# Performance work log

Measured on AMD Instinct MI355X. Metric: run time of the kernel, lower is better.

The kernel has to match this reference:

```python
import jax, jax.numpy as jnp
import numpy as np

EPS = 1e-6
HID = 2048; N_HEADS = 16; Q_LORA = 768; KV_LORA = 512
ROPE_D = 64; NOPE_D = 128; V_D = 128
IDX_H = 32; IDX_D = 128; IDX_TOPK = 512
N_EXP = 8; TOPK = 4; N_GROUP = 4; TOPK_GROUP = 2
MOE_I = 512; SHARED_I = 512; ROUTED_SCALE = 2.5
T = 1024
NEG = -1e30


def _rms(x, w, eps=EPS):
    x = x.astype(jnp.float32)
    return x * jax.lax.rsqrt(jnp.mean(x * x, axis=-1, keepdims=True) + eps) * w


def _ln(x, w, b, eps=EPS):
    x = x.astype(jnp.float32)
    m = jnp.mean(x, axis=-1, keepdims=True)
    v = jnp.mean((x - m) ** 2, axis=-1, keepdims=True)
    return (x - m) * jax.lax.rsqrt(v + eps) * w + b


def _rope_cs(positions, dim):
    inv = 1.0 / (10000.0 ** (jnp.arange(0, dim, 2, dtype=jnp.float32) / dim))
    f = positions.astype(jnp.float32)[:, None] * inv[None, :]  # [T, dim/2]
    return jnp.cos(f), jnp.sin(f)


def _rope(x, cos, sin):
    # neox-style rotate-half over last dim
    d = x.shape[-1] // 2
    x1, x2 = x[..., :d], x[..., d:]
    while cos.ndim < x.ndim:
        cos, sin = cos[:, None], sin[:, None]
    return jnp.concatenate([x1 * cos - x2 * sin, x2 * cos + x1 * sin], axis=-1)


def setup_inputs() -> dict:
    key = jax.random.key(0)
    ks = iter(jax.random.split(key, 32))
    w = lambda *s: jax.random.normal(next(ks), s, jnp.float32) * 0.02
    inp = {
        'positions': jnp.arange(T, dtype=jnp.int32),
        'hidden_states': jax.random.normal(next(ks), (T, HID), jnp.float32),
        'residual': jax.random.normal(next(ks), (T, HID), jnp.float32),
        'w_input_ln': jnp.ones((HID,), jnp.float32),
        'w_post_ln': jnp.ones((HID,), jnp.float32),
        'w_step1': w(Q_LORA + KV_LORA + ROPE_D + IDX_D + IDX_H, HID),
        'w_q_a_ln': jnp.ones((Q_LORA,), jnp.float32),
        'w_kv_a_ln': jnp.ones((KV_LORA,), jnp.float32),
        'idx_k_ln_w': jnp.ones((IDX_D,), jnp.float32),
        'idx_k_ln_b': jnp.zeros((IDX_D,), jnp.float32),
        'w_step3': w(IDX_H * IDX_D + N_HEADS * (NOPE_D + ROPE_D), Q_LORA),
        'W_UK_T': w(N_HEADS, NOPE_D, KV_LORA),
        'W_UV': w(N_HEADS, KV_LORA, V_D),
        'w_o': w(HID, N_HEADS * V_D),
        'gate_w': w(N_EXP, HID),
        'gate_bias': jnp.zeros((N_EXP,), jnp.float32),
        'shared_gate_up': w(2 * SHARED_I, HID),
        'shared_down': w(HID, SHARED_I),
        'exp_gate_up': w(N_EXP, 2 * MOE_I, HID),
        'exp_down': w(N_EXP, HID, MOE_I),
    }
    return inp


def reference(positions, hidden_states, residual, w_input_ln, w_post_ln, w_step1,
              w_q_a_ln, w_kv_a_ln, idx_k_ln_w, idx_k_ln_b, w_step3, W_UK_T, W_UV,
              w_o, gate_w, gate_bias, shared_gate_up, shared_down, exp_gate_up, exp_down):
    Tn = hidden_states.shape[0]
    rows = jnp.arange(Tn)
    # (allreduce is identity at tp=1) + residual add + RMSNorm
    res = hidden_states.astype(jnp.float32) + residual.astype(jnp.float32)
    h = _rms(res, w_input_ln)
    # ---- Step 1: fused qkv_a + indexer_wk + indexer_weights_proj GEMM ----
    s1 = h @ w_step1.T
    o0 = 0
    q_c = s1[:, o0:o0 + Q_LORA]; o0 += Q_LORA
    kv_c = s1[:, o0:o0 + KV_LORA]; o0 += KV_LORA
    k_pe = s1[:, o0:o0 + ROPE_D]; o0 += ROPE_D
    idx_k = s1[:, o0:o0 + IDX_D]; o0 += IDX_D
    idx_w_raw = s1[:, o0:o0 + IDX_H]
    cos, sin = _rope_cs(positions, ROPE_D)
    # fused_norm_rope: norms + rope on k_pe / indexer-k
    q_c = _rms(q_c, w_q_a_ln)
    kv_c = _rms(kv_c, w_kv_a_ln)
    k_pe = _rope(k_pe, cos, sin)
    idx_k = _ln(idx_k, idx_k_ln_w, idx_k_ln_b)
    idx_k = jnp.concatenate([_rope(idx_k[:, :ROPE_D], cos, sin), idx_k[:, ROPE_D:]], axis=-1)
    # ---- Step 3: fused indexer_wq_b + q_b_proj GEMM ----
    s3 = q_c @ w_step3.T
    idx_q = s3[:, :IDX_H * IDX_D].reshape(Tn, IDX_H, IDX_D)
    q = s3[:, IDX_H * IDX_D:].reshape(Tn, N_HEADS, NOPE_D + ROPE_D)
    q_nope, q_pe = q[..., :NOPE_D], q[..., NOPE_D:]
    # absorb W_UK: [T,H,nope] x [H,nope,kv_lora] -> [T,H,kv_lora]
    ql_nope = jnp.einsum('thn,hnk->thk', q_nope, W_UK_T)
    q_pe = _rope(q_pe, cos, sin)
    idx_q = jnp.concatenate([_rope(idx_q[..., :ROPE_D], cos, sin), idx_q[..., ROPE_D:]], axis=-1)
    idx_q = idx_q * (IDX_D ** -0.5)            # indexer softmax scale
    idx_w = idx_w_raw * (IDX_H ** -0.5)        # per-head weights scale
    # ---- sparse attention indexer: relu(q.k) head-weighted sum, causal top-k ----
    il = jnp.einsum('thd,sd->ths', idx_q, idx_k)          # [T,Hi,S]
    iscores = jnp.einsum('ths,th->ts', jax.nn.relu(il), idx_w)
    causal = positions[:, None] >= positions[None, :]
    iscores = jnp.where(causal, iscores, NEG)
    topk_idx = jax.lax.top_k(iscores, IDX_TOPK)[1]        # [T, IDX_TOPK]
    tmask = jnp.zeros((Tn, Tn), bool).at[rows[:, None], topk_idx].set(True)
    mask = causal & tmask
    # ---- MLA MQA attention in latent space ----
    mqa_q = jnp.concatenate([ql_nope, jnp.broadcast_to(q_pe, (Tn, N_HEADS, ROPE_D))], axis=-1)
    kv = jnp.concatenate([kv_c, k_pe], axis=-1)           # [S, kv_lora+rope]
    att = jnp.einsum('thd,sd->hts', mqa_q, kv) * ((NOPE_D + ROPE_D) ** -0.5)
    att = jnp.where(mask[None], att, NEG)
    p = jax.nn.softmax(att, axis=-1)
    o = jnp.einsum('hts,sk->thk', p, kv_c)                # [T,H,kv_lora]
    o = jnp.einsum('thk,hkv->thv', o, W_UV).reshape(Tn, N_HEADS * V_D)
    attn_out = o @ w_o.T
    # add + RMSNorm
    res2 = attn_out + res
    h2 = _rms(res2, w_post_ln)
    # ---- MoE: DeepSeekV3 sigmoid grouped routing + shared experts ----
    glog = h2 @ gate_w.T
    sg = jax.nn.sigmoid(glog)
    sc = sg + gate_bias
    gsz = N_EXP // N_GROUP
    grp = sc.reshape(Tn, N_GROUP, gsz)
    grp_score = jax.lax.top_k(grp, min(2, gsz))[0].sum(-1)
    gidx = jax.lax.top_k(grp_score, TOPK_GROUP)[1]
    gmask = jnp.zeros((Tn, N_GROUP), bool).at[rows[:, None], gidx].set(True)
    emask = jnp.repeat(gmask, gsz, axis=1)
    sc_m = jnp.where(emask, sc, NEG)
    _, tid = jax.lax.top_k(sc_m, TOPK)
    tw = jnp.take_along_axis(sg, tid, axis=1)
    tw = tw / (tw.sum(-1, keepdims=True) + 1e-20) * ROUTED_SCALE
    comb = jnp.zeros((Tn, N_EXP), jnp.float32).at[rows[:, None], tid].set(tw)
    # routed experts (dense masked combine as reference for grouped-GEMM dispatch)
    gu = jnp.einsum('th,eih->tei', h2, exp_gate_up)       # [T,E,2I]
    act = jax.nn.silu(gu[..., :MOE_I]) * gu[..., MOE_I:]
    routed_e = jnp.einsum('tei,ehi->teh', act, exp_down)  # [T,E,H]
    routed = jnp.einsum('te,teh->th', comb, routed_e)
    # shared experts
    gus = h2 @ shared_gate_up.T
    shared = (jax.nn.silu(gus[:, :SHARED_I]) * gus[:, SHARED_I:]) @ shared_down.T
    out = shared + routed
    return out, res2
```

## Files before the change

kernel.cpp:

```cpp
#include <hip/hip_runtime.h>
#include <math.h>

static constexpr int TT  = 1024;
static constexpr int HID = 2048;
static constexpr int NH  = 16;
static constexpr int QL  = 768;
static constexpr int KVL = 512;
static constexpr int RD  = 64;
static constexpr int IH  = 32;
static constexpr int ID  = 128;
static constexpr int S1W = QL + KVL + RD + ID + IH;
static constexpr int S3W = IH*ID + NH*(128+RD);

#define SCALE_ATT 0.07216878364870323f
#define SC_IDXQ   0.08838834764831845f
#define SC_IDXW   0.17677669529663687f
#define NEGR      -1e30f
#define NEGL      -3.0e38f

typedef __bf16 bf16x8 __attribute__((ext_vector_type(8)));
typedef float  f32x4  __attribute__((ext_vector_type(4)));

__device__ __forceinline__ unsigned short f2b(float x) {
  union { float f; unsigned u; } v; v.f = x;
// ... 24 lines not shown
  float vals[8]; float ss = 0.f;
  #pragma unroll
  for (int r = 0; r < 8; r++) {
    int d = threadIdx.x + 256*r;
    float v = hs[(size_t)t*HID + d] + rsd[(size_t)t*HID + d];
    vals[r] = v; res[(size_t)t*HID + d] = v; ss = fmaf(v, v, ss);
  }
  ss = blk_sum256(ss, scr);
  float inv = 1.f/sqrtf(ss/(float)HID + 1e-6f);
  #pragma unroll
  for (int r = 0; r < 8; r++) {
    int d = threadIdx.x + 256*r;
    hb[(size_t)t*HID + d] = f2b(vals[r]*inv*w[d]);
  }
}

__global__ __launch_bounds__(256) void k_res2(const float* __restrict__ attn1,
                                              const float* __restrict__ attn2,
                                              const float* __restrict__ res,
                                              const float* __restrict__ w,
                                              float* __restrict__ res2_out,
                                              float* __restrict__ h2,
                                              unsigned short* __restrict__ h2b) {
  int t = blockIdx.x;
  __shared__ float scr[4];
  float vals[8]; float ss = 0.f;
  #pragma unroll
  for (int r = 0; r < 8; r++) {
    int d = threadIdx.x + 256*r;
    float v = attn1[(size_t)t*HID + d] + attn2[(size_t)t*HID + d] + res[(size_t)t*HID + d];
    vals[r] = v; res2_out[(size_t)t*HID + d] = v; ss = fmaf(v, v, ss);
  }
  ss = blk_sum256(ss, scr);
  float inv = 1.f/sqrtf(ss/(float)HID + 1e-6f);
  #pragma unroll
  for (int r = 0; r < 8; r++) {
    int d = threadIdx.x + 256*r;
    float o = vals[r]*inv*w[d];
    h2[(size_t)t*HID + d] = o;
    h2b[(size_t)t*HID + d] = f2b(o);
  }
}

__global__ void k_ropecs(const int* __restrict__ pos, float* __restrict__ cosb, float* __restrict__ sinb) {
  int i = blockIdx.x*256 + threadIdx.x;
  if (i >= TT*32) return;
  int t = i >> 5, k = i & 31;
  double inv = pow(10000.0, -((double)(2*k))/64.0);
  double f = (double)pos[t] * inv;
  cosb[i] = (float)cos(f);
  sinb[i] = (float)sin(f);
}

__global__ void k_f2b(const float* __restrict__ s, unsigned short* __restrict__ d,
                      long long n, long long ntot) {
  long long stride = (long long)gridDim.x * 1024;
  for (long long i = ((long long)blockIdx.x*256 + threadIdx.x)*4; i < ntot; i += stride) {
    float x0, x1, x2, x3;
    if (i + 3 < n) { float4 v = *(const float4*)(s + i); x0=v.x; x1=v.y; x2=v.z; x3=v.w; }
    else {
      x0 = (i   < n) ? s[i]   : 0.f; x1 = (i+1 < n) ? s[i+1] : 0.f;
      x2 = (i+2 < n) ? s[i+2] : 0.f; x3 = (i+3 < n) ? s[i+3] : 0.f;
    }
    ushort4 o; o.x=f2b(x0); o.y=f2b(x1); o.z=f2b(x2); o.w=f2b(x3);
    *(ushort4*)(d + i) = o;
  }
}

__global__ void k_f2b4(const float* __restrict__ s0, unsigned short* __restrict__ d0, long long n0,
                       const float* __restrict__ s1, unsigned short* __restrict__ d1, long long n1,
                       const float* __restrict__ s2, unsigned short* __restrict__ d2, long long n2,
                       const float* __restrict__ s3, unsigned short* __restrict__ d3, long long n3) {
  long long ntot = n0 + n1 + n2 + n3;
  long long stride = (long long)gridDim.x * 1024;
  for (long long i = ((long long)blockIdx.x*256 + threadIdx.x)*4; i < ntot; i += stride) {
    const float* s; unsigned short* d; long long j = i;
    if (j < n0) { s = s0; d = d0; }
    else { j -= n0;
      if (j < n1) { s = s1; d = d1; }
      else { j -= n1;
        if (j < n2) { s = s2; d = d2; }
        else { j -= n2; s = s3; d = d3; } } }
    float4 v = *(const float4*)(s + j);
    ushort4 o; o.x=f2b(v.x); o.y=f2b(v.y); o.z=f2b(v.z); o.w=f2b(v.w);
    *(ushort4*)(d + j) = o;
  }
}

__global__ __launch_bounds__(256) void k_tconvb(const float* __restrict__ src,
                                                unsigned short* __restrict__ dst,
                                                int R, int C) {
  src += (size_t)blockIdx.z * R * C;
  dst += (size_t)blockIdx.z * R * C;
  __shared__ float tile[32][33];
  int c0 = blockIdx.x * 32, r0 = blockIdx.y * 32;
  int tx = threadIdx.x & 31, ty = threadIdx.x >> 5;
  #pragma unroll
  for (int i = 0; i < 4; i++) {
    int r = r0 + ty + i*8;
    tile[ty + i*8][tx] = src[(size_t)r*C + c0 + tx];
  }
  __syncthreads();
  #pragma unroll
  for (int i = 0; i < 4; i++) {
    int c = c0 + ty + i*8;
    dst[(size_t)c*R + r0 + tx] = f2b(tile[tx][ty + i*8]);
  }
}

template<bool STORE_BF16>
__global__ __launch_bounds__(256) void k_mgemm(const unsigned short* __restrict__ A, int lda, long long sA,
                                               const unsigned short* __restrict__ B, int ldb, long long sB,
                                               void* __restrict__ Cv, int ldc, long long sC,
                                               int N, int K, float alpha, int cskip,
                                               int nseg, long long segA, long long segB) {
  const int row0 = blockIdx.y * 128;
  const int col0 = blockIdx.x * 128;
  if (cskip >= 0 && col0 > row0 + cskip) return;
  __shared__ __align__(16) unsigned short As[128*64];
  __shared__ __align__(16) unsigned short Bs[128*64];
  const int tid  = threadIdx.x;
  const int wave = tid >> 6, lane = tid & 63;
  const int wm = wave >> 1, wn = wave & 1;
  A += (size_t)blockIdx.z * (size_t)sA;
  B += (size_t)blockIdx.z * (size_t)sB;

  f32x4 acc[4][4] = {};

  const int l15 = lane & 15, l4 = lane >> 4;
  const int sx = l15 & 7;

  for (int seg = 0; seg < nseg; seg++) {
    const unsigned short* Ab = A + (size_t)seg * segA;
    const unsigned short* Bb = B + (size_t)seg * segB;
    for (int k0 = 0; k0 < K; k0 += 64) {
      __syncthreads();
      #pragma unroll
      for (int it = 0; it < 4; it++) {
        int sidx = tid + 256*it;
        int r = sidx >> 3, s = sidx & 7;
        int ldsoff = r*64 + ((s ^ (r & 7)) << 3);
        uint4 va = *(const uint4*)(Ab + (size_t)(row0 + r)*lda + k0 + s*8);
        *(uint4*)&As[ldsoff] = va;
        uint4 vb = *(const uint4*)(Bb + (size_t)(col0 + r)*ldb + k0 + s*8);
        *(uint4*)&Bs[ldsoff] = vb;
      }
      __syncthreads();
      #pragma unroll
      for (int kc = 0; kc < 2; kc++) {
        const int sl = ((kc*4 + l4) ^ sx) << 3;
        bf16x8 fa[4], fb[4];
        #pragma unroll
        for (int mf = 0; mf < 4; mf++)
          fa[mf] = *(const bf16x8*)&As[(wm*64 + mf*16 + l15)*64 + sl];
        #pragma unroll
        for (int nf = 0; nf < 4; nf++)
          fb[nf] = *(const bf16x8*)&Bs[(wn*64 + nf*16 + l15)*64 + sl];
        #pragma unroll
        for (int mf = 0; mf < 4; mf++)
          #pragma unroll
          for (int nf = 0; nf < 4; nf++)
            acc[mf][nf] = __builtin_amdgcn_mfma_f32_16x16x32_bf16(fa[mf], fb[nf], acc[mf][nf], 0, 0, 0);
      }
    }
  }

  #pragma unroll
  for (int mf = 0; mf < 4; mf++) {
    #pragma unroll
    for (int nf = 0; nf < 4; nf++) {
      int n = col0 + wn*64 + nf*16 + l15;
      if (n < N) {
        #pragma unroll
        for (int r = 0; r < 4; r++) {
          int m = row0 + wm*64 + mf*16 + l4*4 + r;
          size_t idx = (size_t)m*ldc + n;
          float v = acc[mf][nf][r] * alpha;
          if (STORE_BF16) ((unsigned short*)Cv)[(size_t)blockIdx.z*sC + idx] = f2b(v);
          else            ((float*)Cv)[(size_t)blockIdx.z*sC + idx] = v;
        }
      }
    }
  }
}

__global__ __launch_bounds__(256) void k_post1(const float* __restrict__ s1a,
    const float* __restrict__ s1b,
    const float* __restrict__ wq, const float* __restrict__ wkv,
    const float* __restrict__ lnw, const float* __restrict__ lnb,
    const float* __restrict__ cosb, const float* __restrict__ sinb,
    unsigned short* __restrict__ qcb, float* __restrict__ kvc, float* __restrict__ kpe,
    float* __restrict__ idxk, float* __restrict__ idxw) {
  int t = blockIdx.x, tid = threadIdx.x;
  __shared__ float rowb[S1W];
  __shared__ float scr[4];
  __shared__ float yb[128];
  for (int d = tid; d < S1W; d += 256)
    rowb[d] = s1a[(size_t)t*S1W + d] + s1b[(size_t)t*S1W + d];
  __syncthreads();
  float ss = 0.f;
  for (int d = tid; d < QL; d += 256) { float v = rowb[d]; ss = fmaf(v,v,ss); }
  ss = blk_sum256(ss, scr);
  float inv = 1.f/sqrtf(ss/(float)QL + 1e-6f);
  for (int d = tid; d < QL; d += 256) qcb[(size_t)t*QL + d] = f2b(rowb[d]*inv*wq[d]);
  ss = 0.f;
  for (int d = tid; d < KVL; d += 256) { float v = rowb[QL+d]; ss = fmaf(v,v,ss); }
  ss = blk_sum256(ss, scr);
  inv = 1.f/sqrtf(ss/(float)KVL + 1e-6f);
  for (int d = tid; d < KVL; d += 256) kvc[(size_t)t*KVL + d] = rowb[QL+d]*inv*wkv[d];
  float sm = (tid < 128) ? rowb[1344 + tid] : 0.f;
  float tot = blk_sum256(sm, scr);
  float mean = tot / 128.f;
  float vs = 0.f;
  if (tid < 128) { float v = rowb[1344+tid] - mean; vs = v*v; }
  vs = blk_sum256(vs, scr);
  float ivn = 1.f/sqrtf(vs/128.f + 1e-6f);
  if (tid < 128) yb[tid] = (rowb[1344+tid]-mean)*ivn*lnw[tid] + lnb[tid];
  __syncthreads();
  if (tid < 32) {
    float c = cosb[t*32 + tid], s = sinb[t*32 + tid];
    idxk[(size_t)t*ID + tid]      = yb[tid]*c - yb[32+tid]*s;
    idxk[(size_t)t*ID + 32 + tid] = yb[32+tid]*c + yb[tid]*s;
    float x1 = rowb[1280+tid], x2 = rowb[1312+tid];
    kpe[(size_t)t*RD + tid]      = x1*c - x2*s;
    kpe[(size_t)t*RD + 32 + tid] = x2*c + x1*s;
    idxw[(size_t)t*IH + tid] = rowb[1472+tid] * SC_IDXW;
  } else if (tid >= 64 && tid < 128) {
    idxk[(size_t)t*ID + tid] = yb[tid];
  }
}

__global__ __launch_bounds__(256) void k_post3b(const float* __restrict__ s3,
// ... 67 lines not shown
    float4 v = *(const float4*)(il + (size_t)hh*524288 + (size_t)tr*1024 + s0);
    acc.x += fmaxf(v.x, 0.f) * w;
    acc.y += fmaxf(v.y, 0.f) * w;
    acc.z += fmaxf(v.z, 0.f) * w;
    acc.w += fmaxf(v.w, 0.f) * w;
  }
  if (last) {
    if (s0     > t) acc.x = NEGR;
    if (s0 + 1 > t) acc.y = NEGR;
    if (s0 + 2 > t) acc.z = NEGR;
    if (s0 + 3 > t) acc.w = NEGR;
  }
  *(float4*)(isc + (size_t)tr*TT + s0) = acc;
}

__global__ __launch_bounds__(512) void k_topk(const float* __restrict__ isc,
                                              unsigned char* __restrict__ mask) {
  int t = 512 + blockIdx.x;
  const float* row = isc + (size_t)blockIdx.x * TT;
  __shared__ unsigned long long keys[1024];
  int tid = threadIdx.x;
  for (int i = tid; i < 1024; i += 512) {
    float v = row[i];
    unsigned int b = __float_as_uint(v);
    unsigned int u = (b & 0x80000000u) ? ~b : (b | 0x80000000u);
    keys[i] = ((unsigned long long)u << 32) | (unsigned int)(1023 - i);
  }
  __syncthreads();
  for (int k = 2; k <= 1024; k <<= 1) {
    for (int j = k >> 1; j > 0; j >>= 1) {
      int i = ((tid & ~(j - 1)) << 1) | (tid & (j - 1));
      int l = i | j;
      unsigned long long a = keys[i], b = keys[l];
      bool up = ((i & k) == 0);
      if ((a < b) == up) { keys[i] = b; keys[l] = a; }
      __syncthreads();
    }
  }
  unsigned char* mrow = mask + (size_t)t * TT;
  for (int p = tid; p < 1024; p += 512) {
    int s = 1023 - (int)(keys[p] & 0xFFFFFFFFu);
    mrow[s] = (p < 512) ? (unsigned char)1 : (unsigned char)0;
  }
}

__global__ __launch_bounds__(256) void k_psoft(unsigned short* __restrict__ pb,
                                               const unsigned char* __restrict__ mask) {
  int b = blockIdx.x;
  int t = b & 1023, h = b >> 10;
  unsigned short* row = pb + ((size_t)h << 20) + ((size_t)t << 10);
  int tid = threadIdx.x;
  __shared__ float scr[4];
  int s0 = tid * 4;
  ushort4 raw = *(const ushort4*)(row + s0);
  float v0 = b2f(raw.x), v1 = b2f(raw.y), v2 = b2f(raw.z), v3 = b2f(raw.w);
  bool m0, m1, m2, m3;
  if (t < 512) {
    m0 = (s0 <= t); m1 = (s0+1 <= t); m2 = (s0+2 <= t); m3 = (s0+3 <= t);
  } else {
    uchar4 mk = *(const uchar4*)(mask + (size_t)t*TT + s0);
    m0 = (s0 <= t) && mk.x; m1 = (s0+1 <= t) && mk.y;
    m2 = (s0+2 <= t) && mk.z; m3 = (s0+3 <= t) && mk.w;
  }
  float mx = NEGL;
  if (m0) mx = v0;
  if (m1) mx = fmaxf(mx, v1);
  if (m2) mx = fmaxf(mx, v2);
  if (m3) mx = fmaxf(mx, v3);
  #pragma unroll
  for (int o = 32; o > 0; o >>= 1) mx = fmaxf(mx, __shfl_down(mx, o, 64));
  __syncthreads();
  if ((tid & 63) == 0) scr[tid >> 6] = mx;
  __syncthreads();
  mx = fmaxf(fmaxf(scr[0], scr[1]), fmaxf(scr[2], scr[3]));
  float p0 = m0 ? expf(v0 - mx) : 0.f;
  float p1 = m1 ? expf(v1 - mx) : 0.f;
  float p2 = m2 ? expf(v2 - mx) : 0.f;
  float p3 = m3 ? expf(v3 - mx) : 0.f;
  float sum = blk_sum256((p0+p1)+(p2+p3), scr);
  float inv = 1.f / sum;
  ushort4 o;
  o.x = f2b(p0*inv); o.y = f2b(p1*inv); o.z = f2b(p2*inv); o.w = f2b(p3*inv);
  *(ushort4*)(row + s0) = o;
}

__global__ __launch_bounds__(256) void k_gate(const float* __restrict__ h2,
                                              const float* __restrict__ gw,
                                              const float* __restrict__ gb,
                                              float* __restrict__ comb) {
  int t = blockIdx.x, tid = threadIdx.x;
  int e = tid >> 5, lane = tid & 31;
  __shared__ float gl[8];
  float p = 0.f;
  for (int d = lane; d < HID; d += 32) p = fmaf(h2[(size_t)t*HID+d], gw[(size_t)e*HID+d], p);
  #pragma unroll
  for (int o = 16; o > 0; o >>= 1) p += __shfl_down(p, o, 32);
  if (lane == 0) gl[e] = p;
  __syncthreads();
  if (tid == 0) {
    float sg[8], sc[8];
    #pragma unroll
    for (int i = 0; i < 8; i++) { sg[i] = 1.f/(1.f+expf(-gl[i])); sc[i] = sg[i] + gb[i]; }
    float gs[4];
    #pragma unroll
    for (int g = 0; g < 4; g++) gs[g] = sc[2*g] + sc[2*g+1];
    int g0 = 0;
    for (int g = 1; g < 4; g++) if (gs[g] > gs[g0]) g0 = g;
    int g1 = -1;
    for (int g = 0; g < 4; g++) { if (g == g0) continue; if (g1 < 0 || gs[g] > gs[g1]) g1 = g; }
    float wsum = 1e-20f;
    #pragma unroll
    for (int i = 0; i < 8; i++) { int g = i >> 1; if (g == g0 || g == g1) wsum += sg[i]; }
    #pragma unroll
    for (int i = 0; i < 8; i++) { int g = i >> 1; comb[t*8+i] = (g == g0 || g == g1) ? sg[i]/wsum*2.5f : 0.f; }
  }
}

__global__ void k_swiglu9(const float* __restrict__ gus9, const float* __restrict__ comb,
                          unsigned short* __restrict__ act9) {
  long long i = (long long)blockIdx.x*256 + threadIdx.x;
  int e = (int)(i >> 19);
  int rem = (int)(i & 524287);
  int t = rem >> 9, c = rem & 511;
  const float* g0 = gus9 + (size_t)e*1048576 + (size_t)t*1024;
  float g = g0[c], u = g0[512 + c];
  float w = (e < 8) ? comb[t*8 + e] : 1.f;
  act9[i] = f2b(g/(1.f + expf(-g)) * u * w);
}

__global__ void k_dnred(const float* __restrict__ r, float* __restrict__ o) {
  int i = (blockIdx.x*256 + threadIdx.x)*4;
  float4 a = *(const float4*)(r + i);
  float4 b = *(const float4*)(r + 2097152 + i);
  float4 c = *(const float4*)(r + 4194304 + i);
  float4 v;
  v.x = a.x + b.x + c.x; v.y = a.y + b.y + c.y;
  v.z = a.z + b.z + c.z; v.w = a.w + b.w + c.w;
  *(float4*)(o + i) = v;
}

extern "C" void kernel_launch(void* const* d_in, const int* in_sizes, int n_in,
                              void* d_out, int out_size, void* d_ws, size_t ws_size,
                              hipStream_t stream) {
  const int*   positions = (const int*)d_in[0];
  const float* hs     = (const float*)d_in[1];
  const float* rsd    = (const float*)d_in[2];
  const float* w_in   = (const float*)d_in[3];
  const float* w_post = (const float*)d_in[4];
  const float* w_s1   = (const float*)d_in[5];
  const float* w_qln  = (const float*)d_in[6];
  const float* w_kvln = (const float*)d_in[7];
  const float* iklnw  = (const float*)d_in[8];
  const float* iklnb  = (const float*)d_in[9];
  const float* w_s3   = (const float*)d_in[10];
  const float* wukt   = (const float*)d_in[11];
  const float* wuv    = (const float*)d_in[12];
  const float* w_o    = (const float*)d_in[13];
  const float* gate_w = (const float*)d_in[14];
  const float* gate_b = (const float*)d_in[15];
  const float* sh_gu  = (const float*)d_in[16];
  const float* sh_dn  = (const float*)d_in[17];
  const float* ex_gu  = (const float*)d_in[18];
  const float* ex_dn  = (const float*)d_in[19];

  float* ws = (float*)d_ws;
  typedef unsigned short ush;
  float* RES   = ws + 0;
  float* COSB  = ws + 2097152;
  float* SINB  = ws + 2129920;
  float* KVC   = ws + 2162688;
  float* KPE   = ws + 2686976;
  float* IDXK  = ws + 2752512;
  float* IDXW  = ws + 2883584;
  float* COMB  = ws + 2916352;
  ush*   HB    = (ush*)(ws + 2924544);
  ush*   WS1B  = (ush*)(ws + 3973120);
  float* S1P0  = ws + 5545984;
  ush*   QCB   = (ush*)(ws + 7086080);
  ush*   WS3B  = (ush*)(ws + 7479296);
  ush*   WOB   = (ush*)(ws + 7479296);
  float* S3    = ws + 10231808;
  float* S1P1  = ws + 10231808;
  ush*   S3B   = (ush*)(ws + 17571840);
  ush*   WUKTB = (ush*)(ws + 21241856);
  ush*   QMQAB = (ush*)(ws + 21766144);
  float* ISC   = ws + 26484736;
  unsigned char* MASK = (unsigned char*)(ws + 27009024);
  ush*   WUVB  = (ush*)(ws + 27271168);
  ush*   KVB   = (ush*)(ws + 27795456);
  ush*   VTB   = (ush*)(ws + 28090368);
  ush*   O2B   = (ush*)(ws + 28352512);
  float* ILB   = ws + 27795456;
  ush*   IDXKB = (ush*)(ws + 31989760);
  ush*   PB    = (ush*)(ws + 10231808);
  ush*   OHB   = (ush*)(ws + 18620416);
  float* ATTNP = ws + 10231808;
  float* H2     = ws + 2924544;
  ush*   H2B    = (ush*)(ws + 5021696);
  ush*   EXGUB  = (ush*)(ws + 6070272);
  ush*   SHGUB  = (ush*)(ws + 14458880);
  ush*   EXDNB  = (ush*)(ws + 15507456);
  ush*   SHDNB  = (ush*)(ws + 19701760);
  float* GUS9   = ws + 20226048;
  ush*   ACTB9  = (ush*)(ws + 29663232);
  float* RPART  = ws + 20226048;

  float* OUT0 = (float*)d_out;
  float* OUT_RES2 = OUT0 + (size_t)TT*HID;

  k_prelude<<<TT, 256, 0, stream>>>(hs, rsd, w_in, RES, HB);
  k_ropecs<<<(TT*32)/256, 256, 0, stream>>>(positions, COSB, SINB);
  k_f2b<<<1024, 256, 0, stream>>>(w_s1, WS1B, 3080192LL, 3145728LL);
  k_f2b<<<1024, 256, 0, stream>>>(w_s3, WS3B, 5505024LL, 5505024LL);
  k_tconvb<<<dim3(16,4,16), 256, 0, stream>>>(wukt, WUKTB, 128, 512);
  k_tconvb<<<dim3(4,16,16), 256, 0, stream>>>(wuv, WUVB, 512, 128);
  k_mgemm<false><<<dim3(12,8,2), 256, 0, stream>>>(HB, 2048, 1024, WS1B, 2048, 1024,
                                                   S1P0, S1W, 4685824, 1504, 1024, 1.f, -1, 1, 0, 0);
  k_post1<<<TT, 256, 0, stream>>>(S1P0, S1P1, w_qln, w_kvln, iklnw, iklnb, COSB, SINB, QCB, KVC, KPE, IDXK, IDXW);
  k_f2b<<<128, 256, 0, stream>>>(IDXK, IDXKB, 131072LL, 131072LL);
  k_mgemm<false><<<dim3(56,8,1), 256, 0, stream>>>(QCB, 768, 0, WS3B, 768, 0, S3, S3W, 0, S3W, 768, 1.f, -1, 1, 0, 0);
  k_post3b<<<TT, 256, 0, stream>>>(S3, COSB, SINB, (ush*)S3B);
  k_f2b<<<1024, 256, 0, stream>>>(w_o, WOB, 4194304LL, 4194304LL);
  k_mgemm<true><<<dim3(4,8,16), 256, 0, stream>>>(S3B + 4096, S3W, 192, WUKTB, 128, 65536, QMQAB, 9216, 576, 512, 128, SCALE_ATT, -1, 1, 0, 0);
  k_qpe<<<4096, 256, 0, stream>>>(S3B, QMQAB);
  for (int c = 0; c < 4; c++) {
    k_mgemm<false><<<dim3(8,4,8), 256, 0, stream>>>(S3B + (size_t)512*S3W + c*1024, S3W, 128,
                                                    IDXKB, 128, 0,
                                                    ILB, 1024, 524288,
                                                    1024, 128, 1.f, 639, 1, 0, 0);
    k_ired<<<512, 256, 0, stream>>>(ILB, IDXW, ISC, c == 0, c == 3, c*8);
  }
  k_topk<<<512, 512, 0, stream>>>(ISC, MASK);
  k_kvb<<<2304, 256, 0, stream>>>(KVC, KPE, KVB);
  k_tconvb<<<dim3(16,32,1), 256, 0, stream>>>(KVC, VTB, 1024, 512);
  k_mgemm<true><<<dim3(8,8,16), 256, 0, stream>>>(QMQAB, 9216, 576, KVB, 576, 0, PB, 1024, 1048576, 1024, 576, 1.f, 127, 1, 0, 0);
  k_psoft<<<16384, 256, 0, stream>>>(PB, MASK);
  k_mgemm<true><<<dim3(4,8,16), 256, 0, stream>>>(PB, 1024, 1048576, VTB, 1024, 0, OHB, 512, 524288, 512, 1024, 1.f, -1, 1, 0, 0);
  k_mgemm<true><<<dim3(1,8,16), 256, 0, stream>>>(OHB, 512, 524288, WUVB, 512, 65536, O2B, 2048, 128, 128, 512, 1.f, -1, 1, 0, 0);
  k_mgemm<false><<<dim3(16,8,2), 256, 0, stream>>>(O2B, 2048, 1024, WOB, 2048, 1024,
                                                   ATTNP, 2048, 2097152, 2048, 1024, 1.f, -1, 1, 0, 0);
  k_res2<<<TT, 256, 0, stream>>>(ATTNP, ATTNP + 2097152, RES, w_post, OUT_RES2, H2, H2B);
  k_gate<<<TT, 256, 0, stream>>>(H2, gate_w, gate_b, COMB);
  k_f2b4<<<2048, 256, 0, stream>>>(ex_gu, EXGUB, 16777216LL,
                                   sh_gu, SHGUB, 2097152LL,
                                   ex_dn, EXDNB, 8388608LL,
                                   sh_dn, SHDNB, 1048576LL);
  k_mgemm<false><<<dim3(8,8,9), 256, 0, stream>>>(H2B, 2048, 0, EXGUB, 2048, 2097152, GUS9, 1024, 1048576, 1024, 2048, 1.f, -1, 1, 0, 0);
  k_swiglu9<<<18432, 256, 0, stream>>>(GUS9, COMB, ACTB9);
  k_mgemm<false><<<dim3(16,8,3), 256, 0, stream>>>(ACTB9, 512, 1572864, EXDNB, 512, 3145728,
                                                   RPART, 2048, 2097152, 2048, 512, 1.f, -1, 3, 524288, 1048576);
  k_dnred<<<2048, 256, 0, stream>>>(RPART, OUT0);
}
```

Before: 457.5 us.

## Fuse weight bf16 conversion into GEMM loads, fuse SwiGLU epilogue, skip masked tiles

New measurement: 677.4 us. +48.1%, slower.

```diff
diff --git a/kernel.cpp b/kernel.cpp
--- a/kernel.cpp
+++ b/kernel.cpp
@@ -100,41 +100,6 @@
   sinb[i] = (float)sin(f);
 }
 
-__global__ void k_f2b(const float* __restrict__ s, unsigned short* __restrict__ d,
-                      long long n, long long ntot) {
-  long long stride = (long long)gridDim.x * 1024;
-  for (long long i = ((long long)blockIdx.x*256 + threadIdx.x)*4; i < ntot; i += stride) {
-    float x0, x1, x2, x3;
-    if (i + 3 < n) { float4 v = *(const float4*)(s + i); x0=v.x; x1=v.y; x2=v.z; x3=v.w; }
-    else {
-      x0 = (i   < n) ? s[i]   : 0.f; x1 = (i+1 < n) ? s[i+1] : 0.f;
-      x2 = (i+2 < n) ? s[i+2] : 0.f; x3 = (i+3 < n) ? s[i+3] : 0.f;
-    }
-    ushort4 o; o.x=f2b(x0); o.y=f2b(x1); o.z=f2b(x2); o.w=f2b(x3);
-    *(ushort4*)(d + i) = o;
-  }
-}
-
-__global__ void k_f2b4(const float* __restrict__ s0, unsigned short* __restrict__ d0, long long n0,
-                       const float* __restrict__ s1, unsigned short* __restrict__ d1, long long n1,
-                       const float* __restrict__ s2, unsigned short* __restrict__ d2, long long n2,
-                       const float* __restrict__ s3, unsigned short* __restrict__ d3, long long n3) {
-  long long ntot = n0 + n1 + n2 + n3;
-  long long stride = (long long)gridDim.x * 1024;
-  for (long long i = ((long long)blockIdx.x*256 + threadIdx.x)*4; i < ntot; i += stride) {
-    const float* s; unsigned short* d; long long j = i;
-    if (j < n0) { s = s0; d = d0; }
-    else { j -= n0;
-      if (j < n1) { s = s1; d = d1; }
-      else { j -= n1;
-        if (j < n2) { s = s2; d = d2; }
-        else { j -= n2; s = s3; d = d3; } } }
-    float4 v = *(const float4*)(s + j);
-    ushort4 o; o.x=f2b(v.x); o.y=f2b(v.y); o.z=f2b(v.z); o.w=f2b(v.w);
-    *(ushort4*)(d + j) = o;
-  }
-}
-
 __global__ __launch_bounds__(256) void k_tconvb(const float* __restrict__ src,
                                                 unsigned short* __restrict__ dst,
                                                 int R, int C) {
@@ -156,12 +121,15 @@
   }
 }
 
-template<bool STORE_BF16>
-__global__ __launch_bounds__(256) void k_mgemm(const unsigned short* __restrict__ A, int lda, long long sA,
-                                               const unsigned short* __restrict__ B, int ldb, long long sB,
-                                               void* __restrict__ Cv, int ldc, long long sC,
-                                               int N, int K, float alpha, int cskip,
-                                               int nseg, long long segA, long long segB) {
+template<int OUT, bool BF32, bool ILV>
+__global__ __launch_bounds__(256) void k_mgemm(
+    const unsigned short* __restrict__ A, int lda, long long sA,
+    const void* __restrict__ Bv, const void* __restrict__ B2v,
+    int ldb, long long sB, long long segB, int gz, int b2sw,
+    void* __restrict__ Cv, int ldc, long long sC,
+    int N, int NB, int K, float alpha, int cskip, int ktri,
+    int nseg, long long segA,
+    const float* __restrict__ comb) {
   const int row0 = blockIdx.y * 128;
   const int col0 = blockIdx.x * 128;
   if (cskip >= 0 && col0 > row0 + cskip) return;
@@ -170,18 +138,25 @@
   const int tid  = threadIdx.x;
   const int wave = tid >> 6, lane = tid & 63;
   const int wm = wave >> 1, wn = wave & 1;
-  A += (size_t)blockIdx.z * (size_t)sA;
-  B += (size_t)blockIdx.z * (size_t)sB;
+  const int zb = blockIdx.z;
+  A += (size_t)zb * (size_t)sA;
 
   f32x4 acc[4][4] = {};
-
   const int l15 = lane & 15, l4 = lane >> 4;
   const int sx = l15 & 7;
+  const int Kend = (ktri && K > row0 + 128) ? (row0 + 128) : K;
 
   for (int seg = 0; seg < nseg; seg++) {
     const unsigned short* Ab = A + (size_t)seg * segA;
-    const unsigned short* Bb = B + (size_t)seg * segB;
-    for (int k0 = 0; k0 < K; k0 += 64) {
+    const int g = zb * gz + seg;
+    const float* Bf = nullptr; const unsigned short* Bh = nullptr;
+    if (BF32) {
+      Bf = (g == b2sw) ? (const float*)B2v
+                       : (const float*)Bv + (size_t)zb*sB + (size_t)g*segB;
+    } else {
+      Bh = (const unsigned short*)Bv + (size_t)zb*sB + (size_t)g*segB;
+    }
+    for (int k0 = 0; k0 < Kend; k0 += 64) {
       __syncthreads();
       #pragma unroll
       for (int it = 0; it < 4; it++) {
@@ -190,7 +165,24 @@
         int ldsoff = r*64 + ((s ^ (r & 7)) << 3);
         uint4 va = *(const uint4*)(Ab + (size_t)(row0 + r)*lda + k0 + s*8);
         *(uint4*)&As[ldsoff] = va;
-        uint4 vb = *(const uint4*)(Bb + (size_t)(col0 + r)*ldb + k0 + s*8);
+        int rt = col0 + r;
+        int srow = ILV ? ((rt >> 1) + (rt & 1)*512) : rt;
+        uint4 vb;
+        if (BF32) {
+          if (srow < NB) {
+            const float* bp = Bf + (size_t)srow*ldb + k0 + s*8;
+            float4 f0 = *(const float4*)bp;
+            float4 f1 = *(const float4*)(bp + 4);
+            vb.x = (unsigned)f2b(f0.x) | ((unsigned)f2b(f0.y) << 16);
+            vb.y = (unsigned)f2b(f0.z) | ((unsigned)f2b(f0.w) << 16);
+            vb.z = (unsigned)f2b(f1.x) | ((unsigned)f2b(f1.y) << 16);
+            vb.w = (unsigned)f2b(f1.z) | ((unsigned)f2b(f1.w) << 16);
+          } else {
+            vb = make_uint4(0u, 0u, 0u, 0u);
+          }
+        } else {
+          vb = *(const uint4*)(Bh + (size_t)srow*ldb + k0 + s*8);
+        }
         *(uint4*)&Bs[ldsoff] = vb;
       }
       __syncthreads();
@@ -218,14 +210,21 @@
     #pragma unroll
     for (int nf = 0; nf < 4; nf++) {
       int n = col0 + wn*64 + nf*16 + l15;
-      if (n < N) {
-        #pragma unroll
-        for (int r = 0; r < 4; r++) {
-          int m = row0 + wm*64 + mf*16 + l4*4 + r;
+      #pragma unroll
+      for (int r = 0; r < 4; r++) {
+        int m = row0 + wm*64 + mf*16 + l4*4 + r;
+        float v = acc[mf][nf][r] * alpha;
+        if (OUT == 2) {
+          float p = __shfl_xor(v, 1, 64);
+          if ((l15 & 1) == 0) {
+            float w = (zb < 8) ? comb[m*8 + zb] : 1.f;
+            float rres = v/(1.f + expf(-v)) * p * w;
+            ((unsigned short*)Cv)[(size_t)zb*sC + (size_t)m*ldc + (n >> 1)] = f2b(rres);
+          }
+        } else if (n < N) {
           size_t idx = (size_t)m*ldc + n;
-          float v = acc[mf][nf][r] * alpha;
-          if (STORE_BF16) ((unsigned short*)Cv)[(size_t)blockIdx.z*sC + idx] = f2b(v);
-          else            ((float*)Cv)[(size_t)blockIdx.z*sC + idx] = v;
+          if (OUT == 1) ((unsigned short*)Cv)[(size_t)zb*sC + idx] = f2b(v);
+          else          ((float*)Cv)[(size_t)zb*sC + idx] = v;
         }
       }
     }
@@ -399,15 +398,20 @@
   int tid = threadIdx.x;
   __shared__ float scr[4];
   int s0 = tid * 4;
-  ushort4 raw = *(const ushort4*)(row + s0);
-  float v0 = b2f(raw.x), v1 = b2f(raw.y), v2 = b2f(raw.z), v3 = b2f(raw.w);
-  bool m0, m1, m2, m3;
-  if (t < 512) {
-    m0 = (s0 <= t); m1 = (s0+1 <= t); m2 = (s0+2 <= t); m3 = (s0+3 <= t);
-  } else {
-    uchar4 mk = *(const uchar4*)(mask + (size_t)t*TT + s0);
-    m0 = (s0 <= t) && mk.x; m1 = (s0+1 <= t) && mk.y;
-    m2 = (s0+2 <= t) && mk.z; m3 = (s0+3 <= t) && mk.w;
+  int rub = ((t >> 7) + 1) << 7;
+  bool act = (s0 < rub);
+  float v0 = 0.f, v1 = 0.f, v2 = 0.f, v3 = 0.f;
+  bool m0 = false, m1 = false, m2 = false, m3 = false;
+  if (act) {
+    ushort4 raw = *(const ushort4*)(row + s0);
+    v0 = b2f(raw.x); v1 = b2f(raw.y); v2 = b2f(raw.z); v3 = b2f(raw.w);
+    if (t < 512) {
+      m0 = (s0 <= t); m1 = (s0+1 <= t); m2 = (s0+2 <= t); m3 = (s0+3 <= t);
+    } else {
+      uchar4 mk = *(const uchar4*)(mask + (size_t)t*TT + s0);
+      m0 = (s0 <= t) && mk.x; m1 = (s0+1 <= t) && mk.y;
+      m2 = (s0+2 <= t) && mk.z; m3 = (s0+3 <= t) && mk.w;
+    }
   }
   float mx = NEGL;
   if (m0) mx = v0;
@@ -426,9 +430,11 @@
   float p3 = m3 ? expf(v3 - mx) : 0.f;
   float sum = blk_sum256((p0+p1)+(p2+p3), scr);
   float inv = 1.f / sum;
-  ushort4 o;
-  o.x = f2b(p0*inv); o.y = f2b(p1*inv); o.z = f2b(p2*inv); o.w = f2b(p3*inv);
-  *(ushort4*)(row + s0) = o;
+  if (act) {
+    ushort4 o;
+    o.x = f2b(p0*inv); o.y = f2b(p1*inv); o.z = f2b(p2*inv); o.w = f2b(p3*inv);
+    *(ushort4*)(row + s0) = o;
+  }
 }
 
 __global__ __launch_bounds__(256) void k_gate(const float* __restrict__ h2,
@@ -461,18 +467,6 @@
     #pragma unroll
     for (int i = 0; i < 8; i++) { int g = i >> 1; comb[t*8+i] = (g == g0 || g == g1) ? sg[i]/wsum*2.5f : 0.f; }
   }
-}
-
-__global__ void k_swiglu9(const float* __restrict__ gus9, const float* __restrict__ comb,
-                          unsigned short* __restrict__ act9) {
-  long long i = (long long)blockIdx.x*256 + threadIdx.x;
-  int e = (int)(i >> 19);
-  int rem = (int)(i & 524287);
-  int t = rem >> 9, c = rem & 511;
-  const float* g0 = gus9 + (size_t)e*1048576 + (size_t)t*1024;
-  float g = g0[c], u = g0[512 + c];
-  float w = (e < 8) ? comb[t*8 + e] : 1.f;
-  act9[i] = f2b(g/(1.f + expf(-g)) * u * w);
 }
 
 __global__ void k_dnred(const float* __restrict__ r, float* __restrict__ o) {
@@ -521,13 +515,10 @@
   float* IDXW  = ws + 2883584;
   float* COMB  = ws + 2916352;
   ush*   HB    = (ush*)(ws + 2924544);
-  ush*   WS1B  = (ush*)(ws + 3973120);
-  float* S1P0  = ws + 5545984;
-  ush*   QCB   = (ush*)(ws + 7086080);
-  ush*   WS3B  = (ush*)(ws + 7479296);
-  ush*   WOB   = (ush*)(ws + 7479296);
+  float* S1P0  = ws + 3973120;
+  float* S1P1  = ws + 5513216;
+  ush*   QCB   = (ush*)(ws + 7053312);
   float* S3    = ws + 10231808;
-  float* S1P1  = ws + 10231808;
   ush*   S3B   = (ush*)(ws + 17571840);
   ush*   WUKTB = (ush*)(ws + 21241856);
   ush*   QMQAB = (ush*)(ws + 21766144);
@@ -538,63 +529,62 @@
   ush*   VTB   = (ush*)(ws + 28090368);
   ush*   O2B   = (ush*)(ws + 28352512);
   float* ILB   = ws + 27795456;
-  ush*   IDXKB = (ush*)(ws + 31989760);
   ush*   PB    = (ush*)(ws + 10231808);
   ush*   OHB   = (ush*)(ws + 18620416);
   float* ATTNP = ws + 10231808;
   float* H2     = ws + 2924544;
   ush*   H2B    = (ush*)(ws + 5021696);
-  ush*   EXGUB  = (ush*)(ws + 6070272);
-  ush*   SHGUB  = (ush*)(ws + 14458880);
-  ush*   EXDNB  = (ush*)(ws + 15507456);
-  ush*   SHDNB  = (ush*)(ws + 19701760);
-  float* GUS9   = ws + 20226048;
-  ush*   ACTB9  = (ush*)(ws + 29663232);
-  float* RPART  = ws + 20226048;
+  ush*   ACTB9  = (ush*)(ws + 6070272);
+  float* RPART  = ws + 8429568;
 
   float* OUT0 = (float*)d_out;
   float* OUT_RES2 = OUT0 + (size_t)TT*HID;
 
   k_prelude<<<TT, 256, 0, stream>>>(hs, rsd, w_in, RES, HB);
   k_ropecs<<<(TT*32)/256, 256, 0, stream>>>(positions, COSB, SINB);
-  k_f2b<<<1024, 256, 0, stream>>>(w_s1, WS1B, 3080192LL, 3145728LL);
-  k_f2b<<<1024, 256, 0, stream>>>(w_s3, WS3B, 5505024LL, 5505024LL);
   k_tconvb<<<dim3(16,4,16), 256, 0, stream>>>(wukt, WUKTB, 128, 512);
   k_tconvb<<<dim3(4,16,16), 256, 0, stream>>>(wuv, WUVB, 512, 128);
-  k_mgemm<false><<<dim3(12,8,2), 256, 0, stream>>>(HB, 2048, 1024, WS1B, 2048, 1024,
-                                                   S1P0, S1W, 4685824, 1504, 1024, 1.f, -1, 1, 0, 0);
+  k_mgemm<0,true,false><<<dim3(12,8,2), 256, 0, stream>>>(
+      HB, 2048, 1024, w_s1, nullptr, 2048, 1024, 0, 0, -1,
+      S1P0, S1W, 1540096, 1504, 1504, 1024, 1.f, -1, 0, 1, 0, nullptr);
   k_post1<<<TT, 256, 0, stream>>>(S1P0, S1P1, w_qln, w_kvln, iklnw, iklnb, COSB, SINB, QCB, KVC, KPE, IDXK, IDXW);
-  k_f2b<<<128, 256, 0, stream>>>(IDXK, IDXKB, 131072LL, 131072LL);
-  k_mgemm<false><<<dim3(56,8,1), 256, 0, stream>>>(QCB, 768, 0, WS3B, 768, 0, S3, S3W, 0, S3W, 768, 1.f, -1, 1, 0, 0);
+  k_mgemm<0,true,false><<<dim3(56,8,1), 256, 0, stream>>>(
+      QCB, 768, 0, w_s3, nullptr, 768, 0, 0, 0, -1,
+      S3, S3W, 0, S3W, S3W, 768, 1.f, -1, 0, 1, 0, nullptr);
   k_post3b<<<TT, 256, 0, stream>>>(S3, COSB, SINB, (ush*)S3B);
-  k_f2b<<<1024, 256, 0, stream>>>(w_o, WOB, 4194304LL, 4194304LL);
-  k_mgemm<true><<<dim3(4,8,16), 256, 0, stream>>>(S3B + 4096, S3W, 192, WUKTB, 128, 65536, QMQAB, 9216, 576, 512, 128, SCALE_ATT, -1, 1, 0, 0);
+  k_mgemm<1,false,false><<<dim3(4,8,16), 256, 0, stream>>>(
+      S3B + 4096, S3W, 192, WUKTB, nullptr, 128, 65536, 0, 0, -1,
+      QMQAB, 9216, 576, 512, 512, 128, SCALE_ATT, -1, 0, 1, 0, nullptr);
   k_qpe<<<4096, 256, 0, stream>>>(S3B, QMQAB);
   for (int c = 0; c < 4; c++) {
-    k_mgemm<false><<<dim3(8,4,8), 256, 0, stream>>>(S3B + (size_t)512*S3W + c*1024, S3W, 128,
-                                                    IDXKB, 128, 0,
-                                                    ILB, 1024, 524288,
-                                                    1024, 128, 1.f, 639, 1, 0, 0);
+    k_mgemm<0,true,false><<<dim3(8,4,8), 256, 0, stream>>>(
+        S3B + (size_t)512*S3W + c*1024, S3W, 128, IDXK, nullptr, 128, 0, 0, 0, -1,
+        ILB, 1024, 524288, 1024, 1024, 128, 1.f, 639, 0, 1, 0, nullptr);
     k_ired<<<512, 256, 0, stream>>>(ILB, IDXW, ISC, c == 0, c == 3, c*8);
   }
   k_topk<<<512, 512, 0, stream>>>(ISC, MASK);
   k_kvb<<<2304, 256, 0, stream>>>(KVC, KPE, KVB);
   k_tconvb<<<dim3(16,32,1), 256, 0, stream>>>(KVC, VTB, 1024, 512);
-  k_mgemm<true><<<dim3(8,8,16), 256, 0, stream>>>(QMQAB, 9216, 576, KVB, 576, 0, PB, 1024, 1048576, 1024, 576, 1.f, 127, 1, 0, 0);
+  k_mgemm<1,false,false><<<dim3(8,8,16), 256, 0, stream>>>(
+      QMQAB, 9216, 576, KVB, nullptr, 576, 0, 0, 0, -1,
+      PB, 1024, 1048576, 1024, 1024, 576, 1.f, 127, 0, 1, 0, nullptr);
   k_psoft<<<16384, 256, 0, stream>>>(PB, MASK);
-  k_mgemm<true><<<dim3(4,8,16), 256, 0, stream>>>(PB, 1024, 1048576, VTB, 1024, 0, OHB, 512, 524288, 512, 1024, 1.f, -1, 1, 0, 0);
-  k_mgemm<true><<<dim3(1,8,16), 256, 0, stream>>>(OHB, 512, 524288, WUVB, 512, 65536, O2B, 2048, 128, 128, 512, 1.f, -1, 1, 0, 0);
-  k_mgemm<false><<<dim3(16,8,2), 256, 0, stream>>>(O2B, 2048, 1024, WOB, 2048, 1024,
-                                                   ATTNP, 2048, 2097152, 2048, 1024, 1.f, -1, 1, 0, 0);
+  k_mgemm<1,false,false><<<dim3(4,8,16), 256, 0, stream>>>(
+      PB, 1024, 1048576, VTB, nullptr, 1024, 0, 0, 0, -1,
+      OHB, 512, 524288, 512, 512, 1024, 1.f, -1, 1, 1, 0, nullptr);
+  k_mgemm<1,false,false><<<dim3(1,8,16), 256, 0, stream>>>(
+      OHB, 512, 524288, WUVB, nullptr, 512, 65536, 0, 0, -1,
+      O2B, 2048, 128, 128, 128, 512, 1.f, -1, 0, 1, 0, nullptr);
+  k_mgemm<0,true,false><<<dim3(16,8,2), 256, 0, stream>>>(
+      O2B, 2048, 1024, w_o, nullptr, 2048, 1024, 0, 0, -1,
+      ATTNP, 2048, 2097152, 2048, 2048, 1024, 1.f, -1, 0, 1, 0, nullptr);
   k_res2<<<TT, 256, 0, stream>>>(ATTNP, ATTNP + 2097152, RES, w_post, OUT_RES2, H2, H2B);
   k_gate<<<TT, 256, 0, stream>>>(H2, gate_w, gate_b, COMB);
-  k_f2b4<<<2048, 256, 0, stream>>>(ex_gu, EXGUB, 16777216LL,
-                                   sh_gu, SHGUB, 2097152LL,
-                                   ex_dn, EXDNB, 8388608LL,
-                                   sh_dn, SHDNB, 1048576LL);
-  k_mgemm<false><<<dim3(8,8,9), 256, 0, stream>>>(H2B, 2048, 0, EXGUB, 2048, 2097152, GUS9, 1024, 1048576, 1024, 2048, 1.f, -1, 1, 0, 0);
-  k_swiglu9<<<18432, 256, 0, stream>>>(GUS9, COMB, ACTB9);
-  k_mgemm<false><<<dim3(16,8,3), 256, 0, stream>>>(ACTB9, 512, 1572864, EXDNB, 512, 3145728,
-                                                   RPART, 2048, 2097152, 2048, 512, 1.f, -1, 3, 524288, 1048576);
+  k_mgemm<2,true,true><<<dim3(8,8,9), 256, 0, stream>>>(
+      H2B, 2048, 0, ex_gu, sh_gu, 2048, 0, 2097152, 1, 8,
+      ACTB9, 512, 524288, 1024, 1024, 2048, 1.f, -1, 0, 1, 0, COMB);
+  k_mgemm<0,true,false><<<dim3(16,8,3), 256, 0, stream>>>(
+      ACTB9, 512, 1572864, ex_dn, sh_dn, 512, 0, 1048576, 3, 8,
+      RPART, 2048, 2097152, 2048, 2048, 512, 1.f, -1, 0, 3, 524288, nullptr);
   k_dnred<<<2048, 256, 0, stream>>>(RPART, OUT0);
 }
```

## Fuse SwiGLU into expert gate-up GEMM, skip causal zero work in PV and softmax

Applied to the files above, without the earlier changes.

Result: no change. 454.2 us (-0.7%).

```diff
diff --git a/kernel.cpp b/kernel.cpp
--- a/kernel.cpp
+++ b/kernel.cpp
@@ -156,12 +156,14 @@
   }
 }
 
-template<bool STORE_BF16>
-__global__ __launch_bounds__(256) void k_mgemm(const unsigned short* __restrict__ A, int lda, long long sA,
-                                               const unsigned short* __restrict__ B, int ldb, long long sB,
-                                               void* __restrict__ Cv, int ldc, long long sC,
-                                               int N, int K, float alpha, int cskip,
-                                               int nseg, long long segA, long long segB) {
+template<int OUT, bool ILV>
+__global__ __launch_bounds__(256) void k_mgemm(
+    const unsigned short* __restrict__ A, int lda, long long sA,
+    const unsigned short* __restrict__ B, int ldb, long long sB,
+    void* __restrict__ Cv, int ldc, long long sC,
+    int N, int K, float alpha, int cskip, int ktri,
+    int nseg, long long segA, long long segB,
+    const float* __restrict__ comb) {
   const int row0 = blockIdx.y * 128;
   const int col0 = blockIdx.x * 128;
   if (cskip >= 0 && col0 > row0 + cskip) return;
@@ -170,18 +172,19 @@
   const int tid  = threadIdx.x;
   const int wave = tid >> 6, lane = tid & 63;
   const int wm = wave >> 1, wn = wave & 1;
-  A += (size_t)blockIdx.z * (size_t)sA;
-  B += (size_t)blockIdx.z * (size_t)sB;
+  const int zb = blockIdx.z;
+  A += (size_t)zb * (size_t)sA;
+  B += (size_t)zb * (size_t)sB;
 
   f32x4 acc[4][4] = {};
-
   const int l15 = lane & 15, l4 = lane >> 4;
   const int sx = l15 & 7;
+  const int Kend = (ktri && K > row0 + 128) ? (row0 + 128) : K;
 
   for (int seg = 0; seg < nseg; seg++) {
     const unsigned short* Ab = A + (size_t)seg * segA;
     const unsigned short* Bb = B + (size_t)seg * segB;
-    for (int k0 = 0; k0 < K; k0 += 64) {
+    for (int k0 = 0; k0 < Kend; k0 += 64) {
       __syncthreads();
       #pragma unroll
       for (int it = 0; it < 4; it++) {
@@ -190,7 +193,9 @@
         int ldsoff = r*64 + ((s ^ (r & 7)) << 3);
         uint4 va = *(const uint4*)(Ab + (size_t)(row0 + r)*lda + k0 + s*8);
         *(uint4*)&As[ldsoff] = va;
-        uint4 vb = *(const uint4*)(Bb + (size_t)(col0 + r)*ldb + k0 + s*8);
+        int rt = col0 + r;
+        int srow = ILV ? ((rt >> 1) + (rt & 1)*512) : rt;
+        uint4 vb = *(const uint4*)(Bb + (size_t)srow*ldb + k0 + s*8);
         *(uint4*)&Bs[ldsoff] = vb;
       }
       __syncthreads();
@@ -218,14 +223,21 @@
     #pragma unroll
     for (int nf = 0; nf < 4; nf++) {
       int n = col0 + wn*64 + nf*16 + l15;
-      if (n < N) {
-        #pragma unroll
-        for (int r = 0; r < 4; r++) {
-          int m = row0 + wm*64 + mf*16 + l4*4 + r;
+      #pragma unroll
+      for (int r = 0; r < 4; r++) {
+        int m = row0 + wm*64 + mf*16 + l4*4 + r;
+        float v = acc[mf][nf][r] * alpha;
+        if (OUT == 2) {
+          float p = __shfl_xor(v, 1, 64);
+          if ((l15 & 1) == 0) {
+            float w = (zb < 8) ? comb[m*8 + zb] : 1.f;
+            float rres = v/(1.f + expf(-v)) * p * w;
+            ((unsigned short*)Cv)[(size_t)zb*sC + (size_t)m*ldc + (n >> 1)] = f2b(rres);
+          }
+        } else if (n < N) {
           size_t idx = (size_t)m*ldc + n;
-          float v = acc[mf][nf][r] * alpha;
-          if (STORE_BF16) ((unsigned short*)Cv)[(size_t)blockIdx.z*sC + idx] = f2b(v);
-          else            ((float*)Cv)[(size_t)blockIdx.z*sC + idx] = v;
+          if (OUT == 1) ((unsigned short*)Cv)[(size_t)zb*sC + idx] = f2b(v);
+          else          ((float*)Cv)[(size_t)zb*sC + idx] = v;
         }
       }
     }
@@ -399,15 +411,20 @@
   int tid = threadIdx.x;
   __shared__ float scr[4];
   int s0 = tid * 4;
-  ushort4 raw = *(const ushort4*)(row + s0);
-  float v0 = b2f(raw.x), v1 = b2f(raw.y), v2 = b2f(raw.z), v3 = b2f(raw.w);
-  bool m0, m1, m2, m3;
-  if (t < 512) {
-    m0 = (s0 <= t); m1 = (s0+1 <= t); m2 = (s0+2 <= t); m3 = (s0+3 <= t);
-  } else {
-    uchar4 mk = *(const uchar4*)(mask + (size_t)t*TT + s0);
-    m0 = (s0 <= t) && mk.x; m1 = (s0+1 <= t) && mk.y;
-    m2 = (s0+2 <= t) && mk.z; m3 = (s0+3 <= t) && mk.w;
+  int rub = ((t >> 7) + 1) << 7;
+  bool act = (s0 < rub);
+  float v0 = 0.f, v1 = 0.f, v2 = 0.f, v3 = 0.f;
+  bool m0 = false, m1 = false, m2 = false, m3 = false;
+  if (act) {
+    ushort4 raw = *(const ushort4*)(row + s0);
+    v0 = b2f(raw.x); v1 = b2f(raw.y); v2 = b2f(raw.z); v3 = b2f(raw.w);
+    if (t < 512) {
+      m0 = (s0 <= t); m1 = (s0+1 <= t); m2 = (s0+2 <= t); m3 = (s0+3 <= t);
+    } else {
+      uchar4 mk = *(const uchar4*)(mask + (size_t)t*TT + s0);
+      m0 = (s0 <= t) && mk.x; m1 = (s0+1 <= t) && mk.y;
+      m2 = (s0+2 <= t) && mk.z; m3 = (s0+3 <= t) && mk.w;
+    }
   }
   float mx = NEGL;
   if (m0) mx = v0;
@@ -426,9 +443,11 @@
   float p3 = m3 ? expf(v3 - mx) : 0.f;
   float sum = blk_sum256((p0+p1)+(p2+p3), scr);
   float inv = 1.f / sum;
-  ushort4 o;
-  o.x = f2b(p0*inv); o.y = f2b(p1*inv); o.z = f2b(p2*inv); o.w = f2b(p3*inv);
-  *(ushort4*)(row + s0) = o;
+  if (act) {
+    ushort4 o;
+    o.x = f2b(p0*inv); o.y = f2b(p1*inv); o.z = f2b(p2*inv); o.w = f2b(p3*inv);
+    *(ushort4*)(row + s0) = o;
+  }
 }
 
 __global__ __launch_bounds__(256) void k_gate(const float* __restrict__ h2,
@@ -461,18 +480,6 @@
     #pragma unroll
     for (int i = 0; i < 8; i++) { int g = i >> 1; comb[t*8+i] = (g == g0 || g == g1) ? sg[i]/wsum*2.5f : 0.f; }
   }
-}
-
-__global__ void k_swiglu9(const float* __restrict__ gus9, const float* __restrict__ comb,
-                          unsigned short* __restrict__ act9) {
-  long long i = (long long)blockIdx.x*256 + threadIdx.x;
-  int e = (int)(i >> 19);
-  int rem = (int)(i & 524287);
-  int t = rem >> 9, c = rem & 511;
-  const float* g0 = gus9 + (size_t)e*1048576 + (size_t)t*1024;
-  float g = g0[c], u = g0[512 + c];
-  float w = (e < 8) ? comb[t*8 + e] : 1.f;
-  act9[i] = f2b(g/(1.f + expf(-g)) * u * w);
 }
 
 __global__ void k_dnred(const float* __restrict__ r, float* __restrict__ o) {
@@ -548,9 +555,8 @@
   ush*   SHGUB  = (ush*)(ws + 14458880);
   ush*   EXDNB  = (ush*)(ws + 15507456);
   ush*   SHDNB  = (ush*)(ws + 19701760);
-  float* GUS9   = ws + 20226048;
-  ush*   ACTB9  = (ush*)(ws + 29663232);
-  float* RPART  = ws + 20226048;
+  ush*   ACTB9  = (ush*)(ws + 20226048);
+  float* RPART  = ws + 22585344;
 
   float* OUT0 = (float*)d_out;
   float* OUT_RES2 = OUT0 + (size_t)TT*HID;
@@ -561,40 +567,53 @@
   k_f2b<<<1024, 256, 0, stream>>>(w_s3, WS3B, 5505024LL, 5505024LL);
   k_tconvb<<<dim3(16,4,16), 256, 0, stream>>>(wukt, WUKTB, 128, 512);
   k_tconvb<<<dim3(4,16,16), 256, 0, stream>>>(wuv, WUVB, 512, 128);
-  k_mgemm<false><<<dim3(12,8,2), 256, 0, stream>>>(HB, 2048, 1024, WS1B, 2048, 1024,
-                                                   S1P0, S1W, 4685824, 1504, 1024, 1.f, -1, 1, 0, 0);
+  k_mgemm<0,false><<<dim3(12,8,2), 256, 0, stream>>>(
+      HB, 2048, 1024, WS1B, 2048, 1024, S1P0, S1W, 4685824,
+      1504, 1024, 1.f, -1, 0, 1, 0, 0, nullptr);
   k_post1<<<TT, 256, 0, stream>>>(S1P0, S1P1, w_qln, w_kvln, iklnw, iklnb, COSB, SINB, QCB, KVC, KPE, IDXK, IDXW);
   k_f2b<<<128, 256, 0, stream>>>(IDXK, IDXKB, 131072LL, 131072LL);
-  k_mgemm<false><<<dim3(56,8,1), 256, 0, stream>>>(QCB, 768, 0, WS3B, 768, 0, S3, S3W, 0, S3W, 768, 1.f, -1, 1, 0, 0);
+  k_mgemm<0,false><<<dim3(56,8,1), 256, 0, stream>>>(
+      QCB, 768, 0, WS3B, 768, 0, S3, S3W, 0,
+      S3W, 768, 1.f, -1, 0, 1, 0, 0, nullptr);
   k_post3b<<<TT, 256, 0, stream>>>(S3, COSB, SINB, (ush*)S3B);
   k_f2b<<<1024, 256, 0, stream>>>(w_o, WOB, 4194304LL, 4194304LL);
-  k_mgemm<true><<<dim3(4,8,16), 256, 0, stream>>>(S3B + 4096, S3W, 192, WUKTB, 128, 65536, QMQAB, 9216, 576, 512, 128, SCALE_ATT, -1, 1, 0, 0);
+  k_mgemm<1,false><<<dim3(4,8,16), 256, 0, stream>>>(
+      S3B + 4096, S3W, 192, WUKTB, 128, 65536, QMQAB, 9216, 576,
+      512, 128, SCALE_ATT, -1, 0, 1, 0, 0, nullptr);
   k_qpe<<<4096, 256, 0, stream>>>(S3B, QMQAB);
   for (int c = 0; c < 4; c++) {
-    k_mgemm<false><<<dim3(8,4,8), 256, 0, stream>>>(S3B + (size_t)512*S3W + c*1024, S3W, 128,
-                                                    IDXKB, 128, 0,
-                                                    ILB, 1024, 524288,
-                                                    1024, 128, 1.f, 639, 1, 0, 0);
+    k_mgemm<0,false><<<dim3(8,4,8), 256, 0, stream>>>(
+        S3B + (size_t)512*S3W + c*1024, S3W, 128, IDXKB, 128, 0,
+        ILB, 1024, 524288, 1024, 128, 1.f, 639, 0, 1, 0, 0, nullptr);
     k_ired<<<512, 256, 0, stream>>>(ILB, IDXW, ISC, c == 0, c == 3, c*8);
   }
   k_topk<<<512, 512, 0, stream>>>(ISC, MASK);
   k_kvb<<<2304, 256, 0, stream>>>(KVC, KPE, KVB);
   k_tconvb<<<dim3(16,32,1), 256, 0, stream>>>(KVC, VTB, 1024, 512);
-  k_mgemm<true><<<dim3(8,8,16), 256, 0, stream>>>(QMQAB, 9216, 576, KVB, 576, 0, PB, 1024, 1048576, 1024, 576, 1.f, 127, 1, 0, 0);
+  k_mgemm<1,false><<<dim3(8,8,16), 256, 0, stream>>>(
+      QMQAB, 9216, 576, KVB, 576, 0, PB, 1024, 1048576,
+      1024, 576, 1.f, 127, 0, 1, 0, 0, nullptr);
   k_psoft<<<16384, 256, 0, stream>>>(PB, MASK);
-  k_mgemm<true><<<dim3(4,8,16), 256, 0, stream>>>(PB, 1024, 1048576, VTB, 1024, 0, OHB, 512, 524288, 512, 1024, 1.f, -1, 1, 0, 0);
-  k_mgemm<true><<<dim3(1,8,16), 256, 0, stream>>>(OHB, 512, 524288, WUVB, 512, 65536, O2B, 2048, 128, 128, 512, 1.f, -1, 1, 0, 0);
-  k_mgemm<false><<<dim3(16,8,2), 256, 0, stream>>>(O2B, 2048, 1024, WOB, 2048, 1024,
-                                                   ATTNP, 2048, 2097152, 2048, 1024, 1.f, -1, 1, 0, 0);
+  k_mgemm<1,false><<<dim3(4,8,16), 256, 0, stream>>>(
+      PB, 1024, 1048576, VTB, 1024, 0, OHB, 512, 524288,
+      512, 1024, 1.f, -1, 1, 1, 0, 0, nullptr);
+  k_mgemm<1,false><<<dim3(1,8,16), 256, 0, stream>>>(
+      OHB, 512, 524288, WUVB, 512, 65536, O2B, 2048, 128,
+      128, 512, 1.f, -1, 0, 1, 0, 0, nullptr);
+  k_mgemm<0,false><<<dim3(16,8,2), 256, 0, stream>>>(
+      O2B, 2048, 1024, WOB, 2048, 1024, ATTNP, 2048, 2097152,
+      2048, 1024, 1.f, -1, 0, 1, 0, 0, nullptr);
   k_res2<<<TT, 256, 0, stream>>>(ATTNP, ATTNP + 2097152, RES, w_post, OUT_RES2, H2, H2B);
   k_gate<<<TT, 256, 0, stream>>>(H2, gate_w, gate_b, COMB);
   k_f2b4<<<2048, 256, 0, stream>>>(ex_gu, EXGUB, 16777216LL,
                                    sh_gu, SHGUB, 2097152LL,
                                    ex_dn, EXDNB, 8388608LL,
                                    sh_dn, SHDNB, 1048576LL);
-  k_mgemm<false><<<dim3(8,8,9), 256, 0, stream>>>(H2B, 2048, 0, EXGUB, 2048, 2097152, GUS9, 1024, 1048576, 1024, 2048, 1.f, -1, 1, 0, 0);
-  k_swiglu9<<<18432, 256, 0, stream>>>(GUS9, COMB, ACTB9);
-  k_mgemm<false><<<dim3(16,8,3), 256, 0, stream>>>(ACTB9, 512, 1572864, EXDNB, 512, 3145728,
-                                                   RPART, 2048, 2097152, 2048, 512, 1.f, -1, 3, 524288, 1048576);
+  k_mgemm<2,true><<<dim3(8,8,9), 256, 0, stream>>>(
+      H2B, 2048, 0, EXGUB, 2048, 2097152, ACTB9, 512, 524288,
+      1024, 2048, 1.f, -1, 0, 1, 0, 0, COMB);
+  k_mgemm<0,false><<<dim3(16,8,3), 256, 0, stream>>>(
+      ACTB9, 512, 1572864, EXDNB, 512, 3145728, RPART, 2048, 2097152,
+      2048, 512, 1.f, -1, 0, 3, 524288, 1048576, nullptr);
   k_dnred<<<2048, 256, 0, stream>>>(RPART, OUT0);
 }
```
